# Optimization experiments

Measured on AMD Instinct MI355X. Metric: run time of the kernel, lower is better.

The kernel has to match this reference:

```python
import jax, jax.numpy as jnp
import numpy as np

L, B, D, H, DM = 4, 32768, 64, 256, 32
NS = 8            # fixed RK4 steps standing in for adaptive Dormand-Prince (atol=1e-5)
EPS = 1e-3        # keras BatchNormalization epsilon


def setup_inputs() -> dict:
    key = jax.random.key(0)
    ks = jax.random.split(key, 16)
    g = lambda k, shape, s=0.05: jax.random.normal(k, shape, jnp.float32) * s
    perm = jnp.concatenate([jnp.arange(DM, D), jnp.arange(DM)]).astype(jnp.int32)
    return {
        'x': jax.random.normal(ks[0], (B, D), jnp.float32),
        'perms': jnp.tile(perm[None, :], (L, 1)),
        'nvp_W0': g(ks[1], (L, DM, H)), 'nvp_b0': jnp.zeros((L, H), jnp.float32),
        'nvp_W1': g(ks[2], (L, H, H)), 'nvp_b1': jnp.zeros((L, H), jnp.float32),
        'nvp_W2': g(ks[3], (L, H, 2 * (D - DM))), 'nvp_b2': jnp.zeros((L, 2 * (D - DM)), jnp.float32),
        'ode_W0': g(ks[4], (L, D + 1, H)), 'ode_b0': jnp.zeros((L, H), jnp.float32),
        'ode_W1': g(ks[5], (L, H, H)), 'ode_b1': jnp.zeros((L, H), jnp.float32),
        'ode_W2': g(ks[6], (L, H, D)), 'ode_b2': jnp.zeros((L, D), jnp.float32),
        'bn1_mean': g(ks[7], (L, D), 0.1), 'bn1_var': jax.random.uniform(ks[8], (L, D), jnp.float32, 0.5, 1.5),
        'bn1_gamma': jax.random.uniform(ks[9], (L, D), jnp.float32, 0.8, 1.2), 'bn1_beta': g(ks[10], (L, D), 0.1),
        'bn2_mean': g(ks[11], (L, D), 0.1), 'bn2_var': jax.random.uniform(ks[12], (L, D), jnp.float32, 0.5, 1.5),
        'bn2_gamma': jax.random.uniform(ks[13], (L, D), jnp.float32, 0.8, 1.2), 'bn2_beta': g(ks[14], (L, D), 0.1),
    }


def _nvp(x, W0, b0, W1, b1, W2, b2):
    # RealNVP coupling: pass-through masked half, affine-transform the rest
    x0, x1 = x[:, :DM], x[:, DM:]
    h = jax.nn.relu(x0 @ W0 + b0)
    h = jax.nn.relu(h @ W1 + b1)
    shift, log_scale = jnp.split(h @ W2 + b2, 2, axis=-1)
    return jnp.concatenate([x0, x1 * jnp.exp(log_scale) + shift], axis=-1)


def _bn_fwd(x, mean, var, gamma, beta):
    # TFP BatchNormalization bijector forward == de-normalization
    return (x - beta) * jnp.sqrt(var + EPS) / gamma + mean


def _ffjord(x, W0, b0, W1, b1, W2, b2):
    # integrate dx/dt = MLP([t, x]) from t=0 to t=1 (fixed-step RK4)
    def f(t, y):
        ty = jnp.concatenate([jnp.full((y.shape[0], 1), t, y.dtype), y], axis=-1)
        h = jnp.tanh(ty @ W0 + b0)
        h = jnp.tanh(h @ W1 + b1)
        return h @ W2 + b2

    dt = 1.0 / NS

    def step(y, t):
        k1 = f(t, y)
        k2 = f(t + dt / 2, y + (dt / 2) * k1)
        k3 = f(t + dt / 2, y + (dt / 2) * k2)
        k4 = f(t + dt, y + dt * k3)
        return y + (dt / 6) * (k1 + 2 * k2 + 2 * k3 + k4), None

    ts = jnp.arange(NS, dtype=x.dtype) * dt
    y, _ = jax.lax.scan(step, x, ts)
    return y


def reference(x, perms, nvp_W0, nvp_b0, nvp_W1, nvp_b1, nvp_W2, nvp_b2,
              ode_W0, ode_b0, ode_W1, ode_b1, ode_W2, ode_b2,
              bn1_mean, bn1_var, bn1_gamma, bn1_beta,
              bn2_mean, bn2_var, bn2_gamma, bn2_beta):
    for i in range(L):  # per layer: Permute -> RealNVP -> BN -> FFJORD -> BN
        x = x[:, perms[i]]
        x = _nvp(x, nvp_W0[i], nvp_b0[i], nvp_W1[i], nvp_b1[i], nvp_W2[i], nvp_b2[i])
        x = _bn_fwd(x, bn1_mean[i], bn1_var[i], bn1_gamma[i], bn1_beta[i])
        x = _ffjord(x, ode_W0[i], ode_b0[i], ode_W1[i], ode_b1[i], ode_W2[i], ode_b2[i])
        x = _bn_fwd(x, bn2_mean[i], bn2_var[i], bn2_gamma[i], bn2_beta[i])
    return x
```

## Files before the change

kernel.cpp:

```cpp
#include <hip/hip_runtime.h>
#include <hip/hip_bf16.h>


#define LNUM   4
#define NSTEP  8
#define EPSV   1e-3f

typedef __attribute__((ext_vector_type(8))) short  short8;
typedef __attribute__((ext_vector_type(4))) float  floatx4;

#define MF(a, b, c) __builtin_amdgcn_mfma_f32_16x16x32_bf16((a), (b), (c), 0, 0, 0)

#define OW0_OFF 0
#define OW1_OFF 65536
#define OW2_OFF 327680
#define NW0_OFF 393216
#define NW1_OFF 425984
#define NW2_OFF 688128
#define WS_ELEMS 753664

#define H1_OFF   0
#define H2_OFF   32768
#define YIN_OFF  65536
#define PARS_OFF 73728
#define LDS_SIZE 77056

__device__ __forceinline__ unsigned short f2bfu_rne(float f) {
  unsigned int u = __float_as_uint(f);
  return (unsigned short)((u + 0x7FFFu + ((u >> 16) & 1u)) >> 16);
}

__device__ __forceinline__ unsigned long long pack4bf(float a, float b, float c, float d) {
  __hip_bfloat162 lo = __float22bfloat162_rn(make_float2(a, b));
  __hip_bfloat162 hi = __float22bfloat162_rn(make_float2(c, d));
  unsigned int ul, uh;
  __builtin_memcpy(&ul, &lo, 4);
  __builtin_memcpy(&uh, &hi, 4);
  return (unsigned long long)ul | ((unsigned long long)uh << 32);
}

__device__ __forceinline__ float bfu2f(unsigned short u) {
  return __uint_as_float((unsigned int)u << 16);
}

__device__ __forceinline__ float tanh_fast2(float v) {
  float e = __expf(v);
  return 1.0f - 2.0f * __builtin_amdgcn_rcpf(e + 1.0f);
}

__global__ void prep_kernel(const float* __restrict__ odeW0, const float* __restrict__ odeW1,
                            const float* __restrict__ odeW2, const float* __restrict__ nvpW0,
                            const float* __restrict__ nvpW1, const float* __restrict__ nvpW2,
                            unsigned short* __restrict__ ws) {
  int idx = blockIdx.x * blockDim.x + threadIdx.x;
  if (idx >= WS_ELEMS) return;
  const float* W; int base, K, N, lstride, skip; float scale;
  int f = idx;
  if (f < OW1_OFF)      { W = odeW0; base = OW0_OFF; K = 64;  N = 256; lstride = 16640; skip = 1; scale = 2.f; f -= OW0_OFF; }
  else if (f < OW2_OFF) { W = odeW1; base = OW1_OFF; K = 256; N = 256; lstride = 65536; skip = 0; scale = 2.f; f -= OW1_OFF; }
  else if (f < NW0_OFF) { W = odeW2; base = OW2_OFF; K = 256; N = 64;  lstride = 16384; skip = 0; scale = 1.f; f -= OW2_OFF; }
  else if (f < NW1_OFF) { W = nvpW0; base = NW0_OFF; K = 32;  N = 256; lstride = 8192;  skip = 0; scale = 1.f; f -= NW0_OFF; }
  else if (f < NW2_OFF) { W = nvpW1; base = NW1_OFF; K = 256; N = 256; lstride = 65536; skip = 0; scale = 1.f; f -= NW1_OFF; }
  else                  { W = nvpW2; base = NW2_OFF; K = 256; N = 64;  lstride = 16384; skip = 0; scale = 1.f; f -= NW2_OFF; }
  int per   = K * N;
  int layer = f / per;
  int e     = f - layer * per;
  int j  = e & 7;
  int l  = (e >> 3) & 63;
  int t  = e >> 9;
  int KS = K >> 5; if (KS < 1) KS = 1;
  int ks = t % KS;
  int nt = t / KS;
  int n = nt * 16 + (l & 15);
  int k = ks * 32 + ((l >> 4) << 3) + j;
  ws[base + layer * per + e] = f2bfu_rne(scale * W[layer * lstride + (k + skip) * N + n]);
}

__device__ __forceinline__ void st_h(char* dst, int m, int n0, float a, float b, float c, float d) {
  int off = (m * 512 + n0 * 2) ^ ((m & 15) << 4);
  *reinterpret_cast<unsigned long long*>(dst + off) = pack4bf(a, b, c, d);
}

__global__ void
__launch_bounds__(512)
flow_kernel(const float* __restrict__ xin,
            const float* __restrict__ nvp_b0, const float* __restrict__ nvp_b1,
            const float* __restrict__ nvp_b2,
            const float* __restrict__ odeW0_full,
            const float* __restrict__ ode_b0, const float* __restrict__ ode_b1,
            const float* __restrict__ ode_b2,
            const float* __restrict__ bn1m, const float* __restrict__ bn1v,
            const float* __restrict__ bn1g, const float* __restrict__ bn1b,
            const float* __restrict__ bn2m, const float* __restrict__ bn2v,
            const float* __restrict__ bn2g, const float* __restrict__ bn2b,
            const unsigned short* __restrict__ ws,
            float* __restrict__ out) {
  __shared__ __align__(16) char smem[LDS_SIZE];
  char*  h1   = smem + H1_OFF;
  char*  h2   = smem + H2_OFF;
  char*  yinb = smem + YIN_OFF;
  char*  shfb = smem + H1_OFF;
  float* pars = reinterpret_cast<float*>(smem + PARS_OFF);

  const floatx4 zero4 = {0.f, 0.f, 0.f, 0.f};

  const int tid  = threadIdx.x;
  const int lane = tid & 63;
  const int w    = tid >> 6;
  const int l15  = lane & 15;
  const int g    = lane >> 4;
  const int wn   = w & 3;
  const int wm   = w >> 2;
  const int nb   = w * 32;
  const int row0 = blockIdx.x * 64;
  const int d0   = wn * 16 + g * 4;
  const float dtv = 1.0f / NSTEP;

  float y[8];
  #pragma unroll
  for (int mt = 0; mt < 2; ++mt) {
    int m = wm * 32 + mt * 16 + l15;
    floatx4 v = *reinterpret_cast<const floatx4*>(xin + (row0 + m) * 64 + d0);
    y[mt * 4 + 0] = v[0]; y[mt * 4 + 1] = v[1]; y[mt * 4 + 2] = v[2]; y[mt * 4 + 3] = v[3];
  }

  short8 aw0[2][2];
  short8 aw2h[4];

  for (int l = 0; l < LNUM; ++l) {
    const short8* w1nvp = reinterpret_cast<const short8*>(ws + NW1_OFF + l * 65536);
    const short8* w1ode = reinterpret_cast<const short8*>(ws + OW1_OFF + l * 65536);
    const short8* w2nvp = reinterpret_cast<const short8*>(ws + NW2_OFF + l * 16384);
    const short8* w2ode = reinterpret_cast<const short8*>(ws + OW2_OFF + l * 16384);

    __syncthreads();
    #pragma unroll
    for (int mt = 0; mt < 2; ++mt) {
      int m = wm * 32 + mt * 16 + l15;
      if (wn >= 2) {
        int off = (m * 128 + (d0 - 32) * 2) ^ ((m & 7) << 4);
        *reinterpret_cast<unsigned long long*>(yinb + off) =
            pack4bf(y[mt * 4 + 0], y[mt * 4 + 1], y[mt * 4 + 2], y[mt * 4 + 3]);
      } else {
        int off = (m * 128 + 64 + d0 * 2) ^ ((m & 7) << 4);
        *reinterpret_cast<unsigned long long*>(yinb + off) =
            pack4bf(y[mt * 4 + 0], y[mt * 4 + 1], y[mt * 4 + 2], y[mt * 4 + 3]);
      }
    }
    for (int i = tid; i < 576; i += 512) {
      float v;
      if (i < 256)      v = nvp_b0[l * 256 + i];
      else if (i < 512) v = nvp_b1[l * 256 + i - 256];
      else              v = nvp_b2[l * 64 + i - 512];
      pars[i] = v;
    }
    {
      const short8* p0 = reinterpret_cast<const short8*>(ws + NW0_OFF + l * 8192);
      aw0[0][0] = p0[(w * 2 + 0) * 64 + lane];
      aw0[1][0] = p0[(w * 2 + 1) * 64 + lane];
      #pragma unroll
      for (int ks = 0; ks < 4; ++ks) aw2h[ks] = w2nvp[(wn * 8 + ks) * 64 + lane];
    }
    __syncthreads();

    #pragma unroll
    for (int mh = 0; mh < 2; ++mh) {
      floatx4 acc[2][2];
      #pragma unroll
      for (int nt = 0; nt < 2; ++nt)
        #pragma unroll
        for (int mt = 0; mt < 2; ++mt) acc[nt][mt] = zero4;
      short8 B[2];
      #pragma unroll
      for (int mt = 0; mt < 2; ++mt) {
        int m = mh * 32 + mt * 16 + l15;
        int off = (m * 128 + g * 16) ^ ((m & 7) << 4);
        B[mt] = *reinterpret_cast<const short8*>(yinb + off);
      }
      #pragma unroll
      for (int nt = 0; nt < 2; ++nt)
        #pragma unroll
        for (int mt = 0; mt < 2; ++mt) acc[nt][mt] = MF(aw0[nt][0], B[mt], acc[nt][mt]);
      #pragma unroll
      for (int nt = 0; nt < 2; ++nt) {
        int nbase = nb + nt * 16 + g * 4;
        floatx4 bb = *reinterpret_cast<const floatx4*>(pars + nbase);
        #pragma unroll
        for (int mt = 0; mt < 2; ++mt) {
          int m = mh * 32 + mt * 16 + l15;
          st_h(h1, m, nbase,
               fmaxf(acc[nt][mt][0] + bb[0], 0.f), fmaxf(acc[nt][mt][1] + bb[1], 0.f),
               fmaxf(acc[nt][mt][2] + bb[2], 0.f), fmaxf(acc[nt][mt][3] + bb[3], 0.f));
        }
      }
    }
    __syncthreads();

    #pragma unroll
    for (int mh = 0; mh < 2; ++mh) {
      floatx4 acc[2][2];
      #pragma unroll
      for (int nt = 0; nt < 2; ++nt)
        #pragma unroll
        for (int mt = 0; mt < 2; ++mt) acc[nt][mt] = zero4;
      #pragma unroll
      for (int ks = 0; ks < 8; ++ks) {
        short8 A[2], B[2];
        A[0] = w1nvp[((w * 2 + 0) * 8 + ks) * 64 + lane];
        A[1] = w1nvp[((w * 2 + 1) * 8 + ks) * 64 + lane];
        #pragma unroll
        for (int mt = 0; mt < 2; ++mt) {
          int m = mh * 32 + mt * 16 + l15;
          int off = (m * 512 + (ks * 32 + g * 8) * 2) ^ ((m & 15) << 4);
          B[mt] = *reinterpret_cast<const short8*>(h1 + off);
        }
        #pragma unroll
        for (int nt = 0; nt < 2; ++nt)
          #pragma unroll
          for (int mt = 0; mt < 2; ++mt) acc[nt][mt] = MF(A[nt], B[mt], acc[nt][mt]);
      }
      #pragma unroll
      for (int nt = 0; nt < 2; ++nt) {
        int nbase = nb + nt * 16 + g * 4;
        floatx4 bb = *reinterpret_cast<const floatx4*>(pars + 256 + nbase);
        #pragma unroll
        for (int mt = 0; mt < 2; ++mt) {
          int m = mh * 32 + mt * 16 + l15;
          st_h(h2, m, nbase,
               fmaxf(acc[nt][mt][0] + bb[0], 0.f), fmaxf(acc[nt][mt][1] + bb[1], 0.f),
               fmaxf(acc[nt][mt][2] + bb[2], 0.f), fmaxf(acc[nt][mt][3] + bb[3], 0.f));
        }
      }
    }
    __syncthreads();

    floatx4 a3[2];
    a3[0] = zero4; a3[1] = zero4;
    #pragma unroll
    for (int ks = 0; ks < 8; ++ks) {
      short8 A = (ks < 4) ? aw2h[ks] : w2nvp[(wn * 8 + ks) * 64 + lane];
      #pragma unroll
      for (int mt = 0; mt < 2; ++mt) {
        int m = wm * 32 + mt * 16 + l15;
        int off = (m * 512 + (ks * 32 + g * 8) * 2) ^ ((m & 15) << 4);
        short8 B = *reinterpret_cast<const short8*>(h2 + off);
        a3[mt] = MF(A, B, a3[mt]);
      }
    }
    {
      floatx4 b2v = *reinterpret_cast<const floatx4*>(pars + 512 + d0);
      #pragma unroll
      for (int mt = 0; mt < 2; ++mt)
        #pragma unroll
        for (int p = 0; p < 4; ++p) a3[mt][p] += b2v[p];
    }

    if (wn < 2) {
      #pragma unroll
      for (int mt = 0; mt < 2; ++mt) {
        int m = wm * 32 + mt * 16 + l15;
        int off = (m * 64 + d0 * 2) ^ ((m & 3) << 4);
        *reinterpret_cast<unsigned long long*>(shfb + off) =
            pack4bf(a3[mt][0], a3[mt][1], a3[mt][2], a3[mt][3]);
      }
    }
    __syncthreads();

    #pragma unroll
    for (int mt = 0; mt < 2; ++mt) {
      int m = wm * 32 + mt * 16 + l15;
      if (wn < 2) {
        int off = (m * 128 + d0 * 2) ^ ((m & 7) << 4);
        unsigned long long u = *reinterpret_cast<const unsigned long long*>(yinb + off);
        y[mt * 4 + 0] = bfu2f((unsigned short)(u));
        y[mt * 4 + 1] = bfu2f((unsigned short)(u >> 16));
        y[mt * 4 + 2] = bfu2f((unsigned short)(u >> 32));
        y[mt * 4 + 3] = bfu2f((unsigned short)(u >> 48));
      } else {
        int offx = (m * 128 + 64 + (d0 - 32) * 2) ^ ((m & 7) << 4);
        unsigned long long ux = *reinterpret_cast<const unsigned long long*>(yinb + offx);
        int offs = (m * 64 + (d0 - 32) * 2) ^ ((m & 3) << 4);
        unsigned long long us = *reinterpret_cast<const unsigned long long*>(shfb + offs);
        y[mt * 4 + 0] = bfu2f((unsigned short)(ux)) * __expf(a3[mt][0]) + bfu2f((unsigned short)(us));
        y[mt * 4 + 1] = bfu2f((unsigned short)(ux >> 16)) * __expf(a3[mt][1]) + bfu2f((unsigned short)(us >> 16));
        y[mt * 4 + 2] = bfu2f((unsigned short)(ux >> 32)) * __expf(a3[mt][2]) + bfu2f((unsigned short)(us >> 32));
        y[mt * 4 + 3] = bfu2f((unsigned short)(ux >> 48)) * __expf(a3[mt][3]) + bfu2f((unsigned short)(us >> 48));
      }
    }
    {
      floatx4 mm = *reinterpret_cast<const floatx4*>(bn1m + l * 64 + d0);
      floatx4 vv = *reinterpret_cast<const floatx4*>(bn1v + l * 64 + d0);
      floatx4 gg = *reinterpret_cast<const floatx4*>(bn1g + l * 64 + d0);
      floatx4 be = *reinterpret_cast<const floatx4*>(bn1b + l * 64 + d0);
      float sc[4];
      #pragma unroll
      for (int p = 0; p < 4; ++p) sc[p] = sqrtf(vv[p] + EPSV) / gg[p];
      #pragma unroll
      for (int mt = 0; mt < 2; ++mt)
        #pragma unroll
        for (int p = 0; p < 4; ++p)
          y[mt * 4 + p] = (y[mt * 4 + p] - be[p]) * sc[p] + mm[p];
    }

    for (int i = tid; i < 832; i += 512) {
      float v;
      if (i < 256)      v = 2.f * ode_b0[l * 256 + i];
      else if (i < 512) v = 2.f * ode_b1[l * 256 + i - 256];
      else if (i < 576) v = ode_b2[l * 64 + i - 512];
      else              v = 2.f * odeW0_full[l * 16640 + i - 576];
      pars[i] = v;
    }
    {
      const short8* p0 = reinterpret_cast<const short8*>(ws + OW0_OFF + l * 16384);
      #pragma unroll
      for (int nt = 0; nt < 2; ++nt)
        #pragma unroll
        for (int ks = 0; ks < 2; ++ks) aw0[nt][ks] = p0[((w * 2 + nt) * 2 + ks) * 64 + lane];
      #pragma unroll
      for (int ks = 0; ks < 4; ++ks) aw2h[ks] = w2ode[(wn * 8 + ks) * 64 + lane];
    }
    __syncthreads();

    float ka[8], kc[8];
    for (int s = 0; s < NSTEP; ++s) {
      float t0 = (float)s * dtv;
      for (int stg = 0; stg < 4; ++stg) {
        float cadd = (stg == 0) ? 0.0f : ((stg == 3) ? dtv : 0.5f * dtv);
        float tcur = t0 + cadd;
        #pragma unroll
        for (int mt = 0; mt < 2; ++mt) {
          int m = wm * 32 + mt * 16 + l15;
          float v0, v1, v2, v3;
          if (stg == 0) {
            v0 = y[mt * 4 + 0]; v1 = y[mt * 4 + 1]; v2 = y[mt * 4 + 2]; v3 = y[mt * 4 + 3];
          } else {
            v0 = fmaf(cadd, kc[mt * 4 + 0], y[mt * 4 + 0]);
            v1 = fmaf(cadd, kc[mt * 4 + 1], y[mt * 4 + 1]);
            v2 = fmaf(cadd, kc[mt * 4 + 2], y[mt * 4 + 2]);
            v3 = fmaf(cadd, kc[mt * 4 + 3], y[mt * 4 + 3]);
          }
          int off = (m * 128 + d0 * 2) ^ ((m & 7) << 4);
          *reinterpret_cast<unsigned long long*>(yinb + off) = pack4bf(v0, v1, v2, v3);
        }
        __syncthreads();

        #pragma unroll
        for (int mh = 0; mh < 2; ++mh) {
          floatx4 acc[2][2];
          #pragma unroll
          for (int nt = 0; nt < 2; ++nt)
            #pragma unroll
            for (int mt = 0; mt < 2; ++mt) acc[nt][mt] = zero4;
          #pragma unroll
          for (int ks = 0; ks < 2; ++ks) {
            short8 B[2];
            #pragma unroll
            for (int mt = 0; mt < 2; ++mt) {
              int m = mh * 32 + mt * 16 + l15;
              int off = (m * 128 + (ks * 32 + g * 8) * 2) ^ ((m & 7) << 4);
              B[mt] = *reinterpret_cast<const short8*>(yinb + off);
            }
            #pragma unroll
            for (int nt = 0; nt < 2; ++nt)
              #pragma unroll
              for (int mt = 0; mt < 2; ++mt) acc[nt][mt] = MF(aw0[nt][ks], B[mt], acc[nt][mt]);
          }
          #pragma unroll
          for (int nt = 0; nt < 2; ++nt) {
            int nbase = nb + nt * 16 + g * 4;
            floatx4 bb = *reinterpret_cast<const floatx4*>(pars + nbase);
            floatx4 w0 = *reinterpret_cast<const floatx4*>(pars + 576 + nbase);
            float c0 = bb[0] + tcur * w0[0], c1 = bb[1] + tcur * w0[1];
            float c2 = bb[2] + tcur * w0[2], c3 = bb[3] + tcur * w0[3];
            #pragma unroll
            for (int mt = 0; mt < 2; ++mt) {
              int m = mh * 32 + mt * 16 + l15;
              st_h(h1, m, nbase,
                   tanh_fast2(acc[nt][mt][0] + c0), tanh_fast2(acc[nt][mt][1] + c1),
                   tanh_fast2(acc[nt][mt][2] + c2), tanh_fast2(acc[nt][mt][3] + c3));
            }
          }
        }
        __syncthreads();

        #pragma unroll
        for (int mh = 0; mh < 2; ++mh) {
          floatx4 acc[2][2];
          #pragma unroll
          for (int nt = 0; nt < 2; ++nt)
            #pragma unroll
            for (int mt = 0; mt < 2; ++mt) acc[nt][mt] = zero4;
          #pragma unroll
          for (int ks = 0; ks < 8; ++ks) {
            short8 A[2], B[2];
            A[0] = w1ode[((w * 2 + 0) * 8 + ks) * 64 + lane];
            A[1] = w1ode[((w * 2 + 1) * 8 + ks) * 64 + lane];
            #pragma unroll
            for (int mt = 0; mt < 2; ++mt) {
              int m = mh * 32 + mt * 16 + l15;
              int off = (m * 512 + (ks * 32 + g * 8) * 2) ^ ((m & 15) << 4);
              B[mt] = *reinterpret_cast<const short8*>(h1 + off);
            }
            #pragma unroll
            for (int nt = 0; nt < 2; ++nt)
              #pragma unroll
              for (int mt = 0; mt < 2; ++mt) acc[nt][mt] = MF(A[nt], B[mt], acc[nt][mt]);
          }
          #pragma unroll
          for (int nt = 0; nt < 2; ++nt) {
            int nbase = nb + nt * 16 + g * 4;
            floatx4 bb = *reinterpret_cast<const floatx4*>(pars + 256 + nbase);
            #pragma unroll
            for (int mt = 0; mt < 2; ++mt) {
              int m = mh * 32 + mt * 16 + l15;
              st_h(h2, m, nbase,
                   tanh_fast2(acc[nt][mt][0] + bb[0]), tanh_fast2(acc[nt][mt][1] + bb[1]),
                   tanh_fast2(acc[nt][mt][2] + bb[2]), tanh_fast2(acc[nt][mt][3] + bb[3]));
            }
          }
        }
        __syncthreads();

        {
          floatx4 a2[2];
          a2[0] = zero4; a2[1] = zero4;
          #pragma unroll
          for (int ks = 0; ks < 8; ++ks) {
            short8 A = (ks < 4) ? aw2h[ks] : w2ode[(wn * 8 + ks) * 64 + lane];
            #pragma unroll
            for (int mt = 0; mt < 2; ++mt) {
              int m = wm * 32 + mt * 16 + l15;
              int off = (m * 512 + (ks * 32 + g * 8) * 2) ^ ((m & 15) << 4);
              short8 B = *reinterpret_cast<const short8*>(h2 + off);
              a2[mt] = MF(A, B, a2[mt]);
            }
          }
          floatx4 b2v = *reinterpret_cast<const floatx4*>(pars + 512 + d0);
          #pragma unroll
          for (int mt = 0; mt < 2; ++mt)
            #pragma unroll
            for (int p = 0; p < 4; ++p)
              kc[mt * 4 + p] = a2[mt][p] + b2v[p];
        }
        if (stg == 0) {
          #pragma unroll
          for (int i = 0; i < 8; ++i) ka[i] = kc[i];
        } else if (stg == 3) {
          #pragma unroll
          for (int i = 0; i < 8; ++i) ka[i] += kc[i];
        } else {
          #pragma unroll
          for (int i = 0; i < 8; ++i) ka[i] += 2.0f * kc[i];
        }
      }
      #pragma unroll
      for (int i = 0; i < 8; ++i) y[i] += (dtv / 6.0f) * ka[i];
    }

    {
      floatx4 mm = *reinterpret_cast<const floatx4*>(bn2m + l * 64 + d0);
      floatx4 vv = *reinterpret_cast<const floatx4*>(bn2v + l * 64 + d0);
      floatx4 gg = *reinterpret_cast<const floatx4*>(bn2g + l * 64 + d0);
      floatx4 be = *reinterpret_cast<const floatx4*>(bn2b + l * 64 + d0);
      float sc[4];
      #pragma unroll
      for (int p = 0; p < 4; ++p) sc[p] = sqrtf(vv[p] + EPSV) / gg[p];
      #pragma unroll
      for (int mt = 0; mt < 2; ++mt)
        #pragma unroll
        for (int p = 0; p < 4; ++p)
          y[mt * 4 + p] = (y[mt * 4 + p] - be[p]) * sc[p] + mm[p];
    }
  }

  #pragma unroll
  for (int mt = 0; mt < 2; ++mt) {
    int m = wm * 32 + mt * 16 + l15;
    floatx4 v = {y[mt * 4 + 0], y[mt * 4 + 1], y[mt * 4 + 2], y[mt * 4 + 3]};
    *reinterpret_cast<floatx4*>(out + (row0 + m) * 64 + d0) = v;
  }
}

extern "C" void kernel_launch(void* const* d_in, const int* in_sizes, int n_in,
                              void* d_out, int out_size, void* d_ws, size_t ws_size,
                              hipStream_t stream) {
  const float* x      = (const float*)d_in[0];
  const float* nvpW0  = (const float*)d_in[2];
  const float* nvp_b0 = (const float*)d_in[3];
  const float* nvpW1  = (const float*)d_in[4];
  const float* nvp_b1 = (const float*)d_in[5];
  const float* nvpW2  = (const float*)d_in[6];
  const float* nvp_b2 = (const float*)d_in[7];
  const float* odeW0  = (const float*)d_in[8];
  const float* ode_b0 = (const float*)d_in[9];
  const float* odeW1  = (const float*)d_in[10];
  const float* ode_b1 = (const float*)d_in[11];
  const float* odeW2  = (const float*)d_in[12];
  const float* ode_b2 = (const float*)d_in[13];
  const float* bn1m   = (const float*)d_in[14];
  const float* bn1v   = (const float*)d_in[15];
  const float* bn1g   = (const float*)d_in[16];
  const float* bn1b   = (const float*)d_in[17];
  const float* bn2m   = (const float*)d_in[18];
  const float* bn2v   = (const float*)d_in[19];
  const float* bn2g   = (const float*)d_in[20];
  const float* bn2b   = (const float*)d_in[21];
  unsigned short* ws  = (unsigned short*)d_ws;
  float* out          = (float*)d_out;

  int pblocks = (WS_ELEMS + 255) / 256;
  prep_kernel<<<pblocks, 256, 0, stream>>>(odeW0, odeW1, odeW2, nvpW0, nvpW1, nvpW2, ws);
  flow_kernel<<<512, 512, 0, stream>>>(x, nvp_b0, nvp_b1, nvp_b2, odeW0,
                                       ode_b0, ode_b1, ode_b2,
                                       bn1m, bn1v, bn1g, bn1b,
                                       bn2m, bn2v, bn2g, bn2b,
                                       ws, out);
}
```

Measured before the change: 1.288 ms.

## Shrink blocks to 32 rows with 4 waves, each wave covering full row set

Blocks shrink from 64 rows and 8 waves to 32 rows and 4 waves, with twice as many blocks. Each wave now computes 64 hidden columns across all 32 rows instead of 32 columns for half the rows. LDS use roughly halves, so more blocks can be resident per CU and the 1024-block grid spreads more evenly. The first-layer weights are no longer held in registers and are reloaded from global memory inside the loop, and each weight fragment is now reused over fewer rows, so global weight traffic per row goes up.

```diff
diff --git a/kernel.cpp b/kernel.cpp
--- a/kernel.cpp
+++ b/kernel.cpp
@@ -20,10 +20,10 @@
 #define WS_ELEMS 753664
 
 #define H1_OFF   0
-#define H2_OFF   32768
-#define YIN_OFF  65536
-#define PARS_OFF 73728
-#define LDS_SIZE 77056
+#define H2_OFF   16384
+#define YIN_OFF  32768
+#define PARS_OFF 36864
+#define LDS_SIZE 40192
 
 __device__ __forceinline__ unsigned short f2bfu_rne(float f) {
   unsigned int u = __float_as_uint(f);
@@ -82,7 +82,7 @@
 }
 
 __global__ void
-__launch_bounds__(512)
+__launch_bounds__(256)
 flow_kernel(const float* __restrict__ xin,
             const float* __restrict__ nvp_b0, const float* __restrict__ nvp_b1,
             const float* __restrict__ nvp_b2,
@@ -109,25 +109,24 @@
   const int w    = tid >> 6;
   const int l15  = lane & 15;
   const int g    = lane >> 4;
-  const int wn   = w & 3;
-  const int wm   = w >> 2;
-  const int nb   = w * 32;
-  const int row0 = blockIdx.x * 64;
-  const int d0   = wn * 16 + g * 4;
+  const int nb   = w * 64;
+  const int row0 = blockIdx.x * 32;
+  const int d0   = w * 16 + g * 4;
   const float dtv = 1.0f / NSTEP;
 
   float y[8];
   #pragma unroll
   for (int mt = 0; mt < 2; ++mt) {
-    int m = wm * 32 + mt * 16 + l15;
+    int m = mt * 16 + l15;
     floatx4 v = *reinterpret_cast<const floatx4*>(xin + (row0 + m) * 64 + d0);
     y[mt * 4 + 0] = v[0]; y[mt * 4 + 1] = v[1]; y[mt * 4 + 2] = v[2]; y[mt * 4 + 3] = v[3];
   }
 
-  short8 aw0[2][2];
   short8 aw2h[4];
 
   for (int l = 0; l < LNUM; ++l) {
+    const short8* w0nvp = reinterpret_cast<const short8*>(ws + NW0_OFF + l * 8192);
+    const short8* w0ode = reinterpret_cast<const short8*>(ws + OW0_OFF + l * 16384);
     const short8* w1nvp = reinterpret_cast<const short8*>(ws + NW1_OFF + l * 65536);
     const short8* w1ode = reinterpret_cast<const short8*>(ws + OW1_OFF + l * 65536);
     const short8* w2nvp = reinterpret_cast<const short8*>(ws + NW2_OFF + l * 16384);
@@ -136,8 +135,8 @@
     __syncthreads();
     #pragma unroll
     for (int mt = 0; mt < 2; ++mt) {
-      int m = wm * 32 + mt * 16 + l15;
-      if (wn >= 2) {
+      int m = mt * 16 + l15;
+      if (w >= 2) {
         int off = (m * 128 + (d0 - 32) * 2) ^ ((m & 7) << 4);
         *reinterpret_cast<unsigned long long*>(yinb + off) =
             pack4bf(y[mt * 4 + 0], y[mt * 4 + 1], y[mt * 4 + 2], y[mt * 4 + 3]);
@@ -147,47 +146,43 @@
             pack4bf(y[mt * 4 + 0], y[mt * 4 + 1], y[mt * 4 + 2], y[mt * 4 + 3]);
       }
     }
-    for (int i = tid; i < 576; i += 512) {
+    for (int i = tid; i < 576; i += 256) {
       float v;
       if (i < 256)      v = nvp_b0[l * 256 + i];
       else if (i < 512) v = nvp_b1[l * 256 + i - 256];
       else              v = nvp_b2[l * 64 + i - 512];
       pars[i] = v;
     }
+    #pragma unroll
+    for (int ks = 0; ks < 4; ++ks) aw2h[ks] = w2nvp[(w * 8 + ks) * 64 + lane];
+    __syncthreads();
+
     {
-      const short8* p0 = reinterpret_cast<const short8*>(ws + NW0_OFF + l * 8192);
-      aw0[0][0] = p0[(w * 2 + 0) * 64 + lane];
-      aw0[1][0] = p0[(w * 2 + 1) * 64 + lane];
-      #pragma unroll
-      for (int ks = 0; ks < 4; ++ks) aw2h[ks] = w2nvp[(wn * 8 + ks) * 64 + lane];
-    }
-    __syncthreads();
-
-    #pragma unroll
-    for (int mh = 0; mh < 2; ++mh) {
-      floatx4 acc[2][2];
-      #pragma unroll
-      for (int nt = 0; nt < 2; ++nt)
+      floatx4 acc[4][2];
+      #pragma unroll
+      for (int nt = 0; nt < 4; ++nt)
         #pragma unroll
         for (int mt = 0; mt < 2; ++mt) acc[nt][mt] = zero4;
       short8 B[2];
       #pragma unroll
       for (int mt = 0; mt < 2; ++mt) {
-        int m = mh * 32 + mt * 16 + l15;
+        int m = mt * 16 + l15;
         int off = (m * 128 + g * 16) ^ ((m & 7) << 4);
         B[mt] = *reinterpret_cast<const short8*>(yinb + off);
       }
       #pragma unroll
-      for (int nt = 0; nt < 2; ++nt)
-        #pragma unroll
-        for (int mt = 0; mt < 2; ++mt) acc[nt][mt] = MF(aw0[nt][0], B[mt], acc[nt][mt]);
-      #pragma unroll
-      for (int nt = 0; nt < 2; ++nt) {
+      for (int nt = 0; nt < 4; ++nt) {
+        short8 A = w0nvp[(w * 4 + nt) * 64 + lane];
+        #pragma unroll
+        for (int mt = 0; mt < 2; ++mt) acc[nt][mt] = MF(A, B[mt], acc[nt][mt]);
+      }
+      #pragma unroll
+      for (int nt = 0; nt < 4; ++nt) {
         int nbase = nb + nt * 16 + g * 4;
         floatx4 bb = *reinterpret_cast<const floatx4*>(pars + nbase);
         #pragma unroll
         for (int mt = 0; mt < 2; ++mt) {
-          int m = mh * 32 + mt * 16 + l15;
+          int m = mt * 16 + l15;
           st_h(h1, m, nbase,
                fmaxf(acc[nt][mt][0] + bb[0], 0.f), fmaxf(acc[nt][mt][1] + bb[1], 0.f),
                fmaxf(acc[nt][mt][2] + bb[2], 0.f), fmaxf(acc[nt][mt][3] + bb[3], 0.f));
@@ -196,36 +191,35 @@
     }
     __syncthreads();
 
-    #pragma unroll
-    for (int mh = 0; mh < 2; ++mh) {
-      floatx4 acc[2][2];
-      #pragma unroll
-      for (int nt = 0; nt < 2; ++nt)
+    {
+      floatx4 acc[4][2];
+      #pragma unroll
+      for (int nt = 0; nt < 4; ++nt)
         #pragma unroll
         for (int mt = 0; mt < 2; ++mt) acc[nt][mt] = zero4;
       #pragma unroll
       for (int ks = 0; ks < 8; ++ks) {
-        short8 A[2], B[2];
-        A[0] = w1nvp[((w * 2 + 0) * 8 + ks) * 64 + lane];
-        A[1] = w1nvp[((w * 2 + 1) * 8 + ks) * 64 + lane];
+        short8 B[2];
         #pragma unroll
         for (int mt = 0; mt < 2; ++mt) {
-          int m = mh * 32 + mt * 16 + l15;
+          int m = mt * 16 + l15;
           int off = (m * 512 + (ks * 32 + g * 8) * 2) ^ ((m & 15) << 4);
           B[mt] = *reinterpret_cast<const short8*>(h1 + off);
         }
         #pragma unroll
-        for (int nt = 0; nt < 2; ++nt)
-          #pragma unroll
-          for (int mt = 0; mt < 2; ++mt) acc[nt][mt] = MF(A[nt], B[mt], acc[nt][mt]);
-      }
-      #pragma unroll
-      for (int nt = 0; nt < 2; ++nt) {
+        for (int nt = 0; nt < 4; ++nt) {
+          short8 A = w1nvp[((w * 4 + nt) * 8 + ks) * 64 + lane];
+          #pragma unroll
+          for (int mt = 0; mt < 2; ++mt) acc[nt][mt] = MF(A, B[mt], acc[nt][mt]);
+        }
+      }
+      #pragma unroll
+      for (int nt = 0; nt < 4; ++nt) {
         int nbase = nb + nt * 16 + g * 4;
         floatx4 bb = *reinterpret_cast<const floatx4*>(pars + 256 + nbase);
         #pragma unroll
         for (int mt = 0; mt < 2; ++mt) {
-          int m = mh * 32 + mt * 16 + l15;
+          int m = mt * 16 + l15;
           st_h(h2, m, nbase,
                fmaxf(acc[nt][mt][0] + bb[0], 0.f), fmaxf(acc[nt][mt][1] + bb[1], 0.f),
                fmaxf(acc[nt][mt][2] + bb[2], 0.f), fmaxf(acc[nt][mt][3] + bb[3], 0.f));
@@ -238,10 +232,10 @@
     a3[0] = zero4; a3[1] = zero4;
     #pragma unroll
     for (int ks = 0; ks < 8; ++ks) {
-      short8 A = (ks < 4) ? aw2h[ks] : w2nvp[(wn * 8 + ks) * 64 + lane];
+      short8 A = (ks < 4) ? aw2h[ks] : w2nvp[(w * 8 + ks) * 64 + lane];
       #pragma unroll
       for (int mt = 0; mt < 2; ++mt) {
-        int m = wm * 32 + mt * 16 + l15;
+        int m = mt * 16 + l15;
         int off = (m * 512 + (ks * 32 + g * 8) * 2) ^ ((m & 15) << 4);
         short8 B = *reinterpret_cast<const short8*>(h2 + off);
         a3[mt] = MF(A, B, a3[mt]);
@@ -255,10 +249,10 @@
         for (int p = 0; p < 4; ++p) a3[mt][p] += b2v[p];
     }
 
-    if (wn < 2) {
+    if (w < 2) {
       #pragma unroll
       for (int mt = 0; mt < 2; ++mt) {
-        int m = wm * 32 + mt * 16 + l15;
+        int m = mt * 16 + l15;
         int off = (m * 64 + d0 * 2) ^ ((m & 3) << 4);
         *reinterpret_cast<unsigned long long*>(shfb + off) =
             pack4bf(a3[mt][0], a3[mt][1], a3[mt][2], a3[mt][3]);
@@ -268,8 +262,8 @@
 
     #pragma unroll
     for (int mt = 0; mt < 2; ++mt) {
-      int m = wm * 32 + mt * 16 + l15;
-      if (wn < 2) {
+      int m = mt * 16 + l15;
+      if (w < 2) {
         int off = (m * 128 + d0 * 2) ^ ((m & 7) << 4);
         unsigned long long u = *reinterpret_cast<const unsigned long long*>(yinb + off);
         y[mt * 4 + 0] = bfu2f((unsigned short)(u));
@@ -302,7 +296,7 @@
           y[mt * 4 + p] = (y[mt * 4 + p] - be[p]) * sc[p] + mm[p];
     }
 
-    for (int i = tid; i < 832; i += 512) {
+    for (int i = tid; i < 832; i += 256) {
       float v;
       if (i < 256)      v = 2.f * ode_b0[l * 256 + i];
       else if (i < 512) v = 2.f * ode_b1[l * 256 + i - 256];
@@ -310,15 +304,8 @@
       else              v = 2.f * odeW0_full[l * 16640 + i - 576];
       pars[i] = v;
     }
-    {
-      const short8* p0 = reinterpret_cast<const short8*>(ws + OW0_OFF + l * 16384);
-      #pragma unroll
-      for (int nt = 0; nt < 2; ++nt)
-        #pragma unroll
-        for (int ks = 0; ks < 2; ++ks) aw0[nt][ks] = p0[((w * 2 + nt) * 2 + ks) * 64 + lane];
-      #pragma unroll
-      for (int ks = 0; ks < 4; ++ks) aw2h[ks] = w2ode[(wn * 8 + ks) * 64 + lane];
-    }
+    #pragma unroll
+    for (int ks = 0; ks < 4; ++ks) aw2h[ks] = w2ode[(w * 8 + ks) * 64 + lane];
     __syncthreads();
 
     float ka[8], kc[8];
@@ -329,7 +316,7 @@
         float tcur = t0 + cadd;
         #pragma unroll
         for (int mt = 0; mt < 2; ++mt) {
-          int m = wm * 32 + mt * 16 + l15;
+          int m = mt * 16 + l15;
           float v0, v1, v2, v3;
           if (stg == 0) {
             v0 = y[mt * 4 + 0]; v1 = y[mt * 4 + 1]; v2 = y[mt * 4 + 2]; v3 = y[mt * 4 + 3];
@@ -344,11 +331,10 @@
         }
         __syncthreads();
 
-        #pragma unroll
-        for (int mh = 0; mh < 2; ++mh) {
-          floatx4 acc[2][2];
-          #pragma unroll
-          for (int nt = 0; nt < 2; ++nt)
+        {
+          floatx4 acc[4][2];
+          #pragma unroll
+          for (int nt = 0; nt < 4; ++nt)
             #pragma unroll
             for (int mt = 0; mt < 2; ++mt) acc[nt][mt] = zero4;
           #pragma unroll
@@ -356,17 +342,19 @@
             short8 B[2];
             #pragma unroll
             for (int mt = 0; mt < 2; ++mt) {
-              int m = mh * 32 + mt * 16 + l15;
+              int m = mt * 16 + l15;
               int off = (m * 128 + (ks * 32 + g * 8) * 2) ^ ((m & 7) << 4);
               B[mt] = *reinterpret_cast<const short8*>(yinb + off);
             }
             #pragma unroll
-            for (int nt = 0; nt < 2; ++nt)
+            for (int nt = 0; nt < 4; ++nt) {
+              short8 A = w0ode[((w * 4 + nt) * 2 + ks) * 64 + lane];
               #pragma unroll
-              for (int mt = 0; mt < 2; ++mt) acc[nt][mt] = MF(aw0[nt][ks], B[mt], acc[nt][mt]);
+              for (int mt = 0; mt < 2; ++mt) acc[nt][mt] = MF(A, B[mt], acc[nt][mt]);
+            }
           }
           #pragma unroll
-          for (int nt = 0; nt < 2; ++nt) {
+          for (int nt = 0; nt < 4; ++nt) {
             int nbase = nb + nt * 16 + g * 4;
             floatx4 bb = *reinterpret_cast<const floatx4*>(pars + nbase);
             floatx4 w0 = *reinterpret_cast<const floatx4*>(pars + 576 + nbase);
@@ -374,7 +362,7 @@
             float c2 = bb[2] + tcur * w0[2], c3 = bb[3] + tcur * w0[3];
             #pragma unroll
             for (int mt = 0; mt < 2; ++mt) {
-              int m = mh * 32 + mt * 16 + l15;
+              int m = mt * 16 + l15;
               st_h(h1, m, nbase,
                    tanh_fast2(acc[nt][mt][0] + c0), tanh_fast2(acc[nt][mt][1] + c1),
                    tanh_fast2(acc[nt][mt][2] + c2), tanh_fast2(acc[nt][mt][3] + c3));
@@ -383,36 +371,35 @@
         }
         __syncthreads();
 
-        #pragma unroll
-        for (int mh = 0; mh < 2; ++mh) {
-          floatx4 acc[2][2];
-          #pragma unroll
-          for (int nt = 0; nt < 2; ++nt)
+        {
+          floatx4 acc[4][2];
+          #pragma unroll
+          for (int nt = 0; nt < 4; ++nt)
             #pragma unroll
             for (int mt = 0; mt < 2; ++mt) acc[nt][mt] = zero4;
           #pragma unroll
           for (int ks = 0; ks < 8; ++ks) {
-            short8 A[2], B[2];
-            A[0] = w1ode[((w * 2 + 0) * 8 + ks) * 64 + lane];
-            A[1] = w1ode[((w * 2 + 1) * 8 + ks) * 64 + lane];
+            short8 B[2];
             #pragma unroll
             for (int mt = 0; mt < 2; ++mt) {
-              int m = mh * 32 + mt * 16 + l15;
+              int m = mt * 16 + l15;
               int off = (m * 512 + (ks * 32 + g * 8) * 2) ^ ((m & 15) << 4);
               B[mt] = *reinterpret_cast<const short8*>(h1 + off);
             }
             #pragma unroll
-            for (int nt = 0; nt < 2; ++nt)
+            for (int nt = 0; nt < 4; ++nt) {
+              short8 A = w1ode[((w * 4 + nt) * 8 + ks) * 64 + lane];
               #pragma unroll
-              for (int mt = 0; mt < 2; ++mt) acc[nt][mt] = MF(A[nt], B[mt], acc[nt][mt]);
+              for (int mt = 0; mt < 2; ++mt) acc[nt][mt] = MF(A, B[mt], acc[nt][mt]);
+            }
           }
           #pragma unroll
-          for (int nt = 0; nt < 2; ++nt) {
+          for (int nt = 0; nt < 4; ++nt) {
             int nbase = nb + nt * 16 + g * 4;
             floatx4 bb = *reinterpret_cast<const floatx4*>(pars + 256 + nbase);
             #pragma unroll
             for (int mt = 0; mt < 2; ++mt) {
-              int m = mh * 32 + mt * 16 + l15;
+              int m = mt * 16 + l15;
               st_h(h2, m, nbase,
                    tanh_fast2(acc[nt][mt][0] + bb[0]), tanh_fast2(acc[nt][mt][1] + bb[1]),
                    tanh_fast2(acc[nt][mt][2] + bb[2]), tanh_fast2(acc[nt][mt][3] + bb[3]));
@@ -426,10 +413,10 @@
           a2[0] = zero4; a2[1] = zero4;
           #pragma unroll
           for (int ks = 0; ks < 8; ++ks) {
-            short8 A = (ks < 4) ? aw2h[ks] : w2ode[(wn * 8 + ks) * 64 + lane];
+            short8 A = (ks < 4) ? aw2h[ks] : w2ode[(w * 8 + ks) * 64 + lane];
             #pragma unroll
             for (int mt = 0; mt < 2; ++mt) {
-              int m = wm * 32 + mt * 16 + l15;
+              int m = mt * 16 + l15;
               int off = (m * 512 + (ks * 32 + g * 8) * 2) ^ ((m & 15) << 4);
               short8 B = *reinterpret_cast<const short8*>(h2 + off);
               a2[mt] = MF(A, B, a2[mt]);
@@ -475,7 +462,7 @@
 
   #pragma unroll
   for (int mt = 0; mt < 2; ++mt) {
-    int m = wm * 32 + mt * 16 + l15;
+    int m = mt * 16 + l15;
     floatx4 v = {y[mt * 4 + 0], y[mt * 4 + 1], y[mt * 4 + 2], y[mt * 4 + 3]};
     *reinterpret_cast<floatx4*>(out + (row0 + m) * 64 + d0) = v;
   }
@@ -510,9 +497,9 @@
 
   int pblocks = (WS_ELEMS + 255) / 256;
   prep_kernel<<<pblocks, 256, 0, stream>>>(odeW0, odeW1, odeW2, nvpW0, nvpW1, nvpW2, ws);
-  flow_kernel<<<512, 512, 0, stream>>>(x, nvp_b0, nvp_b1, nvp_b2, odeW0,
-                                       ode_b0, ode_b1, ode_b2,
-                                       bn1m, bn1v, bn1g, bn1b,
-                                       bn2m, bn2v, bn2g, bn2b,
-                                       ws, out);
-}
+  flow_kernel<<<1024, 256, 0, stream>>>(x, nvp_b0, nvp_b1, nvp_b2, odeW0,
+                                        ode_b0, ode_b1, ode_b2,
+                                        bn1m, bn1v, bn1g, bn1b,
+                                        bn2m, bn2v, bn2g, bn2b,
+                                        ws, out);
+}
```

Result: slower. 1.863 ms (+44.6%).
